# Performance work log

Hardware: AMD Instinct MI355X
Metric: run time of the kernel (lower is better)

The kernel has to match this reference:

```python
import jax, jax.numpy as jnp
from jax import lax
import numpy as np

B, L, CV = 64, 196, 2048
T = 20
VOCAB, E, H, A = 10000, 512, 512, 512


def setup_inputs() -> dict:
    key = jax.random.key(0)
    ks = jax.random.split(key, 16)
    s = 0.02
    return {
        "V": jax.random.normal(ks[0], (B, L, CV), jnp.float32),
        "caps": jax.random.randint(ks[1], (B, T), 0, VOCAB, jnp.int32),
        "embed_W": jax.random.normal(ks[2], (VOCAB, E), jnp.float32) * s,
        "Wh_w": jax.random.normal(ks[3], (A, H), jnp.float32) * s,
        "Wh_b": jnp.zeros((A,), jnp.float32),
        "Wv_w": jax.random.normal(ks[4], (A, CV), jnp.float32) * s,
        "Wv_b": jnp.zeros((A,), jnp.float32),
        "v_w": jax.random.normal(ks[5], (1, A), jnp.float32) * s,
        "v_b": jnp.zeros((1,), jnp.float32),
        "W_ih": jax.random.normal(ks[6], (4 * H, E + CV), jnp.float32) * s,
        "W_hh": jax.random.normal(ks[7], (4 * H, H), jnp.float32) * s,
        "b_ih": jnp.zeros((4 * H,), jnp.float32),
        "b_hh": jnp.zeros((4 * H,), jnp.float32),
        "out_w": jax.random.normal(ks[8], (VOCAB, H), jnp.float32) * s,
        "out_b": jnp.zeros((VOCAB,), jnp.float32),
    }


def reference(V, caps, embed_W, Wh_w, Wh_b, Wv_w, Wv_b, v_w, v_b,
              W_ih, W_hh, b_ih, b_hh, out_w, out_b):
    Bv = V.shape[0]
    Tc = caps.shape[1]
    Hd = W_hh.shape[1]
    emb = embed_W[caps]  # [B,T,E]
    # attention keys over image regions are constant across timesteps
    k = jnp.einsum('blc,ac->bla', V, Wv_w) + Wv_b  # [B,L,A]
    h0 = jnp.zeros((Bv, Hd), V.dtype)
    c0 = jnp.zeros((Bv, Hd), V.dtype)

    def step(carry, yprev):
        h, c = carry
        # additive attention
        q = h @ Wh_w.T + Wh_b                                  # [B,A]
        e = jnp.einsum('bla,a->bl', jnp.tanh(q[:, None, :] + k), v_w[0]) + v_b[0]
        a = jax.nn.softmax(e, axis=-1)                         # [B,L]
        ctx = jnp.einsum('bl,blc->bc', a, V)                   # [B,CV]
        # LSTMCell
        x = jnp.concatenate([yprev, ctx], axis=-1)             # [B,E+CV]
        gates = x @ W_ih.T + b_ih + h @ W_hh.T + b_hh          # [B,4H]
        i, f, g, o = jnp.split(gates, 4, axis=-1)
        c_new = jax.nn.sigmoid(f) * c + jax.nn.sigmoid(i) * jnp.tanh(g)
        h_new = jax.nn.sigmoid(o) * jnp.tanh(c_new)
        logits = h_new @ out_w.T + out_b                       # [B,VOCAB]
        return (h_new, c_new), logits

    xs = jnp.transpose(emb[:, :Tc - 1, :], (1, 0, 2))          # [T-1,B,E]
    _, logits = lax.scan(step, (h0, c0), xs)                   # [T-1,B,VOCAB]
    return jnp.transpose(logits, (1, 0, 2))                    # [B,T-1,VOCAB]
```

## Files before the change

kernel.cpp:

```cpp
#include <hip/hip_runtime.h>


typedef __bf16 bf16x8 __attribute__((ext_vector_type(8)));
typedef float f32x4 __attribute__((ext_vector_type(4)));
typedef unsigned short ushort8 __attribute__((ext_vector_type(8)));

#define OFF_HALL 0ull
#define OFF_X2H  622592ull
#define OFF_H    704512ull
#define OFF_C    737280ull
#define OFF_QP   770048ull
#define OFF_PART 901120ull
#define OFF_AB   1425408ull

#define D_WGH 0ull
#define D_GE  2621440ull
#define D_KB  5111808ull

__device__ __forceinline__ unsigned short f2bf(float f) {
    unsigned int u = __float_as_uint(f);
    unsigned int r = u + 0x7FFFu + ((u >> 16) & 1u);
    return (unsigned short)(r >> 16);
}
__device__ __forceinline__ float bf2f(unsigned short h) {
    return __uint_as_float(((unsigned int)h) << 16);
}
__device__ __forceinline__ float ftanh(float x) {
    x = fminf(fmaxf(x, -15.f), 15.f);
    float e = __expf(2.f * x);
    return (e - 1.f) / (e + 1.f);
}
__device__ __forceinline__ float fsig(float x) {
    x = fminf(fmaxf(x, -30.f), 30.f);
    return 1.f / (1.f + __expf(-x));
}

__global__ void init_state(float* __restrict__ ws) {
    const int b = blockIdx.x, tid = threadIdx.x;
    float* h  = ws + OFF_H;
    float* c  = ws + OFF_C;
    unsigned short* x2h = (unsigned short*)(ws + OFF_X2H);
    for (int j = tid; j < 512; j += 256) {
        h[b * 512 + j] = 0.f;
        c[b * 512 + j] = 0.f;
        x2h[b * 2560 + 2048 + j] = 0;
    }
}

__global__ __launch_bounds__(256)
void conv_wg(const float* __restrict__ Wih, const float* __restrict__ Whh,
             unsigned short* __restrict__ Wgh) {
    const int idx = blockIdx.x * 256 + threadIdx.x;
    const int j = idx / 320;
    const int c0 = (idx - j * 320) * 8;
    const float* src;
    if (c0 < 2048) src = Wih + (size_t)j * 2560 + 512 + c0;
    else           src = Whh + (size_t)j * 512 + (c0 - 2048);
    float4 a = *reinterpret_cast<const float4*>(src);
    float4 b = *reinterpret_cast<const float4*>(src + 4);
    ushort8 o;
    o[0]=f2bf(a.x); o[1]=f2bf(a.y); o[2]=f2bf(a.z); o[3]=f2bf(a.w);
    o[4]=f2bf(b.x); o[5]=f2bf(b.y); o[6]=f2bf(b.z); o[7]=f2bf(b.w);
    *reinterpret_cast<ushort8*>(Wgh + (size_t)j * 2560 + c0) = o;
}

__global__ __launch_bounds__(256)
void gemm_k_mfma(const float* __restrict__ V, const float* __restrict__ Wv,
                 const float* __restrict__ bv, unsigned short* __restrict__ kout) {
    __shared__ unsigned short At[64 * 32];
    __shared__ unsigned short Bt[64 * 32];
    const int tid = threadIdx.x;
    const int lane = tid & 63, wave = tid >> 6;
    const int wr = wave >> 1, wc = wave & 1;
    const int m0 = blockIdx.x * 64, n0 = blockIdx.y * 64;
    const int srow = tid >> 2, skg = tid & 3;
    const float* ga = V  + (size_t)(m0 + srow) * 2048 + skg * 8;
    const float* gb = Wv + (size_t)(n0 + srow) * 2048 + skg * 8;
    const int ar0 = (wr * 32 + (lane & 15)) * 32 + (lane >> 4) * 8;
    const int br0 = (wc * 32 + (lane & 15)) * 32 + (lane >> 4) * 8;
    f32x4 acc[2][2] = {};
    for (int k0 = 0; k0 < 2048; k0 += 32) {
        float4 a0 = *reinterpret_cast<const float4*>(ga + k0);
        float4 a1 = *reinterpret_cast<const float4*>(ga + k0 + 4);
        float4 b0 = *reinterpret_cast<const float4*>(gb + k0);
        float4 b1 = *reinterpret_cast<const float4*>(gb + k0 + 4);
        ushort8 ua, ub;
        ua[0]=f2bf(a0.x); ua[1]=f2bf(a0.y); ua[2]=f2bf(a0.z); ua[3]=f2bf(a0.w);
        ua[4]=f2bf(a1.x); ua[5]=f2bf(a1.y); ua[6]=f2bf(a1.z); ua[7]=f2bf(a1.w);
        ub[0]=f2bf(b0.x); ub[1]=f2bf(b0.y); ub[2]=f2bf(b0.z); ub[3]=f2bf(b0.w);
        ub[4]=f2bf(b1.x); ub[5]=f2bf(b1.y); ub[6]=f2bf(b1.z); ub[7]=f2bf(b1.w);
        *reinterpret_cast<ushort8*>(&At[tid * 8]) = ua;
        *reinterpret_cast<ushort8*>(&Bt[tid * 8]) = ub;
        __syncthreads();
        bf16x8 af0 = *reinterpret_cast<const bf16x8*>(&At[ar0]);
        bf16x8 af1 = *reinterpret_cast<const bf16x8*>(&At[ar0 + 16 * 32]);
        bf16x8 bf0 = *reinterpret_cast<const bf16x8*>(&Bt[br0]);
        bf16x8 bf1 = *reinterpret_cast<const bf16x8*>(&Bt[br0 + 16 * 32]);
        acc[0][0] = __builtin_amdgcn_mfma_f32_16x16x32_bf16(af0, bf0, acc[0][0], 0, 0, 0);
        acc[0][1] = __builtin_amdgcn_mfma_f32_16x16x32_bf16(af0, bf1, acc[0][1], 0, 0, 0);
        acc[1][0] = __builtin_amdgcn_mfma_f32_16x16x32_bf16(af1, bf0, acc[1][0], 0, 0, 0);
        acc[1][1] = __builtin_amdgcn_mfma_f32_16x16x32_bf16(af1, bf1, acc[1][1], 0, 0, 0);
        __syncthreads();
    }
#pragma unroll
    for (int fi = 0; fi < 2; ++fi)
#pragma unroll
        for (int fj = 0; fj < 2; ++fj)
#pragma unroll
            for (int r = 0; r < 4; ++r) {
                int m = m0 + wr * 32 + fi * 16 + (lane >> 4) * 4 + r;
                int n = n0 + wc * 32 + fj * 16 + (lane & 15);
                kout[(size_t)m * 512 + n] = f2bf(acc[fi][fj][r] + bv[n]);
            }
}

__global__ __launch_bounds__(256)
void gemm_emb(const float* __restrict__ embW, const int* __restrict__ caps,
              const float* __restrict__ Wih, const float* __restrict__ bih,
              const float* __restrict__ bhh, float* __restrict__ ge) {
    const int t = blockIdx.x;
    const int n0 = blockIdx.y * 64;
    __shared__ float As[32][68];
    __shared__ float Bs[32][68];
    __shared__ int capss[64];
    const int tid = threadIdx.x;
    const int tx = tid & 15, ty = tid >> 4;
    if (tid < 64) capss[tid] = caps[tid * 20 + t];
    __syncthreads();
    float acc[4][4] = {{0.f}};
    for (int k0 = 0; k0 < 512; k0 += 32) {
#pragma unroll
        for (int i = 0; i < 2; ++i) {
            int idx = tid + i * 256;
            int m = idx >> 3, cc = idx & 7;
            float4 av = *reinterpret_cast<const float4*>(embW + (size_t)capss[m] * 512 + k0 + cc * 4);
            As[cc * 4 + 0][m] = av.x; As[cc * 4 + 1][m] = av.y;
            As[cc * 4 + 2][m] = av.z; As[cc * 4 + 3][m] = av.w;
            float4 bw = *reinterpret_cast<const float4*>(Wih + (size_t)(n0 + m) * 2560 + k0 + cc * 4);
            Bs[cc * 4 + 0][m] = bw.x; Bs[cc * 4 + 1][m] = bw.y;
            Bs[cc * 4 + 2][m] = bw.z; Bs[cc * 4 + 3][m] = bw.w;
        }
        __syncthreads();
#pragma unroll
        for (int kk = 0; kk < 32; ++kk) {
            float4 a4 = *reinterpret_cast<const float4*>(&As[kk][ty * 4]);
            float4 b4 = *reinterpret_cast<const float4*>(&Bs[kk][tx * 4]);
            float ar[4] = {a4.x, a4.y, a4.z, a4.w};
            float br[4] = {b4.x, b4.y, b4.z, b4.w};
#pragma unroll
            for (int i2 = 0; i2 < 4; ++i2)
#pragma unroll
                for (int j2 = 0; j2 < 4; ++j2)
                    acc[i2][j2] = fmaf(ar[i2], br[j2], acc[i2][j2]);
        }
        __syncthreads();
    }
#pragma unroll
    for (int i2 = 0; i2 < 4; ++i2) {
        int m = ty * 4 + i2;
        int n = n0 + tx * 4;
        float4 o;
        o.x = acc[i2][0] + bih[n + 0] + bhh[n + 0];
        o.y = acc[i2][1] + bih[n + 1] + bhh[n + 1];
        o.z = acc[i2][2] + bih[n + 2] + bhh[n + 2];
        o.w = acc[i2][3] + bih[n + 3] + bhh[n + 3];
        *reinterpret_cast<float4*>(ge + (size_t)(t * 64 + m) * 2048 + n) = o;
    }
}

__global__ __launch_bounds__(256)
void kq_gemm(const float* __restrict__ Whw, float* __restrict__ ws) {
    const float* h = ws + OFF_H;
    float* qp = ws + OFF_QP;
    const int n0 = blockIdx.x * 64;
    const int kc = blockIdx.y;
    __shared__ float As[32][68];
    __shared__ float Bs[32][68];
    const int tid = threadIdx.x;
    const int tx = tid & 15, ty = tid >> 4;
    float acc[4][4] = {{0.f}};
    for (int kt = 0; kt < 4; ++kt) {
        int kb = kc * 128 + kt * 32;
#pragma unroll
        for (int i = 0; i < 2; ++i) {
            int idx = tid + i * 256;
            int m = idx >> 3, cc = idx & 7;
            float4 av = *reinterpret_cast<const float4*>(h + (size_t)m * 512 + kb + cc * 4);
            As[cc * 4 + 0][m] = av.x; As[cc * 4 + 1][m] = av.y;
            As[cc * 4 + 2][m] = av.z; As[cc * 4 + 3][m] = av.w;
            float4 bw = *reinterpret_cast<const float4*>(Whw + (size_t)(n0 + m) * 512 + kb + cc * 4);
            Bs[cc * 4 + 0][m] = bw.x; Bs[cc * 4 + 1][m] = bw.y;
            Bs[cc * 4 + 2][m] = bw.z; Bs[cc * 4 + 3][m] = bw.w;
        }
        __syncthreads();
#pragma unroll
        for (int kk = 0; kk < 32; ++kk) {
            float4 a4 = *reinterpret_cast<const float4*>(&As[kk][ty * 4]);
            float4 b4 = *reinterpret_cast<const float4*>(&Bs[kk][tx * 4]);
            float ar[4] = {a4.x, a4.y, a4.z, a4.w};
            float br[4] = {b4.x, b4.y, b4.z, b4.w};
#pragma unroll
            for (int i2 = 0; i2 < 4; ++i2)
#pragma unroll
                for (int j2 = 0; j2 < 4; ++j2)
                    acc[i2][j2] = fmaf(ar[i2], br[j2], acc[i2][j2]);
        }
        __syncthreads();
    }
#pragma unroll
    for (int i2 = 0; i2 < 4; ++i2) {
        int b = ty * 4 + i2;
        int n = n0 + tx * 4;
        float4 o = make_float4(acc[i2][0], acc[i2][1], acc[i2][2], acc[i2][3]);
        *reinterpret_cast<float4*>(qp + (size_t)(kc * 64 + b) * 512 + n) = o;
    }
}

__global__ __launch_bounds__(256)
void attn_step(const float* __restrict__ Whb, const float* __restrict__ vw,
               const unsigned short* __restrict__ kb, float* __restrict__ ws) {
    const int b = blockIdx.x, tid = threadIdx.x;
    const float* qp = ws + OFF_QP;
    float* abuf = ws + OFF_AB;
    __shared__ float qs[512];
    __shared__ float es[196];
    __shared__ float red[256];
    for (int j = tid; j < 512; j += 256) {
        float q = Whb[j];
#pragma unroll
        for (int p = 0; p < 4; ++p) q += qp[(size_t)(p * 64 + b) * 512 + j];
        qs[j] = q;
    }
    __syncthreads();
    const int w = tid >> 6, lane = tid & 63;
    float qr[8], vr[8];
#pragma unroll
    for (int j = 0; j < 8; ++j) {
        qr[j] = qs[lane * 8 + j];
        vr[j] = vw[lane * 8 + j];
    }
    for (int l = w; l < 196; l += 4) {
        const unsigned short* kr = kb + (size_t)(b * 196 + l) * 512 + lane * 8;
        ushort8 kv = *reinterpret_cast<const ushort8*>(kr);
        float s = 0.f;
#pragma unroll
        for (int j = 0; j < 8; ++j)
            s += vr[j] * ftanh(qr[j] + bf2f(kv[j]));
#pragma unroll
        for (int mm = 32; mm >= 1; mm >>= 1) s += __shfl_xor(s, mm);
        if (lane == 0) es[l] = s;
    }
    __syncthreads();
    float ev = (tid < 196) ? es[tid] : -1e30f;
    red[tid] = ev;
    __syncthreads();
    for (int s2 = 128; s2 > 0; s2 >>= 1) {
        if (tid < s2) red[tid] = fmaxf(red[tid], red[tid + s2]);
        __syncthreads();
    }
    float mx = red[0];
    __syncthreads();
    float p = (tid < 196) ? __expf(ev - mx) : 0.f;
    red[tid] = p;
    __syncthreads();
    for (int s2 = 128; s2 > 0; s2 >>= 1) {
        if (tid < s2) red[tid] += red[tid + s2];
        __syncthreads();
    }
    if (tid < 196) abuf[b * 196 + tid] = p / red[0];
}

__global__ __launch_bounds__(256)
void ctx_wide(const float* __restrict__ V, float* __restrict__ ws) {
    const int b = blockIdx.y, tid = threadIdx.x;
    const int c = blockIdx.x * 256 + tid;
    const float* abuf = ws + OFF_AB;
    unsigned short* x2h = (unsigned short*)(ws + OFF_X2H);
    __shared__ float as_[196];
    if (tid < 196) as_[tid] = abuf[b * 196 + tid];
    __syncthreads();
    const float* vb = V + (size_t)b * 196 * 2048 + c;
    float a0 = 0.f, a1 = 0.f, a2 = 0.f, a3 = 0.f;
    for (int l = 0; l < 196; l += 4) {
        a0 = fmaf(as_[l + 0], vb[(size_t)(l + 0) * 2048], a0);
        a1 = fmaf(as_[l + 1], vb[(size_t)(l + 1) * 2048], a1);
        a2 = fmaf(as_[l + 2], vb[(size_t)(l + 2) * 2048], a2);
        a3 = fmaf(as_[l + 3], vb[(size_t)(l + 3) * 2048], a3);
    }
    x2h[(size_t)b * 2560 + c] = f2bf((a0 + a1) + (a2 + a3));
}

__global__ __launch_bounds__(256)
void gates_mfma(const float* __restrict__ ws, const unsigned short* __restrict__ Wgh,
                float* __restrict__ part_out) {
    __shared__ unsigned short At[64 * 32];
    __shared__ unsigned short Bt[64 * 32];
    const unsigned short* x2h = (const unsigned short*)(ws + OFF_X2H);
    const int tid = threadIdx.x;
    const int lane = tid & 63, wave = tid >> 6;
    const int wr = wave >> 1, wc = wave & 1;
    const int n0 = blockIdx.x * 64;
    const int kc = blockIdx.y;
    const int srow = tid >> 2, skg = tid & 3;
    const unsigned short* ga = x2h + (size_t)srow * 2560 + kc * 640 + skg * 8;
    const unsigned short* gb = Wgh + (size_t)(n0 + srow) * 2560 + kc * 640 + skg * 8;
    const int ar0 = (wr * 32 + (lane & 15)) * 32 + (lane >> 4) * 8;
    const int br0 = (wc * 32 + (lane & 15)) * 32 + (lane >> 4) * 8;
    f32x4 acc[2][2] = {};
    for (int kt = 0; kt < 20; ++kt) {
        *reinterpret_cast<ushort8*>(&At[tid * 8]) = *reinterpret_cast<const ushort8*>(ga + kt * 32);
        *reinterpret_cast<ushort8*>(&Bt[tid * 8]) = *reinterpret_cast<const ushort8*>(gb + kt * 32);
        __syncthreads();
        bf16x8 af0 = *reinterpret_cast<const bf16x8*>(&At[ar0]);
        bf16x8 af1 = *reinterpret_cast<const bf16x8*>(&At[ar0 + 16 * 32]);
        bf16x8 bf0 = *reinterpret_cast<const bf16x8*>(&Bt[br0]);
        bf16x8 bf1 = *reinterpret_cast<const bf16x8*>(&Bt[br0 + 16 * 32]);
        acc[0][0] = __builtin_amdgcn_mfma_f32_16x16x32_bf16(af0, bf0, acc[0][0], 0, 0, 0);
        acc[0][1] = __builtin_amdgcn_mfma_f32_16x16x32_bf16(af0, bf1, acc[0][1], 0, 0, 0);
        acc[1][0] = __builtin_amdgcn_mfma_f32_16x16x32_bf16(af1, bf0, acc[1][0], 0, 0, 0);
        acc[1][1] = __builtin_amdgcn_mfma_f32_16x16x32_bf16(af1, bf1, acc[1][1], 0, 0, 0);
        __syncthreads();
    }
#pragma unroll
    for (int fi = 0; fi < 2; ++fi)
#pragma unroll
        for (int fj = 0; fj < 2; ++fj)
#pragma unroll
            for (int r = 0; r < 4; ++r) {
                int m = wr * 32 + fi * 16 + (lane >> 4) * 4 + r;
                int n = n0 + wc * 32 + fj * 16 + (lane & 15);
                part_out[(size_t)(kc * 64 + m) * 2048 + n] = acc[fi][fj][r];
            }
}

__global__ __launch_bounds__(256)
void lstm_step(float* __restrict__ ws, const float* __restrict__ geb, int t) {
    const int b = blockIdx.x, tid = threadIdx.x;
    const float* ge = geb + (size_t)(t * 64 + b) * 2048;
    const float* part = ws + OFF_PART;
    float* h = ws + OFF_H;
    float* c = ws + OFF_C;
    unsigned short* x2h = (unsigned short*)(ws + OFF_X2H);
    float* hall = ws + OFF_HALL;
#pragma unroll
    for (int jj = 0; jj < 2; ++jj) {
        int j = tid + jj * 256;
        float ig = ge[j], fg = ge[512 + j], gg = ge[1024 + j], og = ge[1536 + j];
#pragma unroll
        for (int p = 0; p < 4; ++p) {
            const float* pp = part + (size_t)(p * 64 + b) * 2048;
            ig += pp[j]; fg += pp[512 + j]; gg += pp[1024 + j]; og += pp[1536 + j];
        }
        float cv = fsig(fg) * c[b * 512 + j] + fsig(ig) * ftanh(gg);
        float hv = fsig(og) * ftanh(cv);
        c[b * 512 + j] = cv;
        h[b * 512 + j] = hv;
        x2h[(size_t)b * 2560 + 2048 + j] = f2bf(hv);
        hall[(size_t)(t * 64 + b) * 512 + j] = hv;
    }
}

__global__ __launch_bounds__(256)
void gemm_logits_mfma(const float* __restrict__ outw, const float* __restrict__ outb,
                      const float* __restrict__ ws, float* __restrict__ out) {
    __shared__ unsigned short At[64 * 32];
    __shared__ unsigned short Bt[64 * 32];
    const float* hall = ws + OFF_HALL;
    const int tid = threadIdx.x;
    const int lane = tid & 63, wave = tid >> 6;
    const int wr = wave >> 1, wc = wave & 1;
    const int t = blockIdx.x;
    const int n0 = blockIdx.y * 64;
    const int srow = tid >> 2, skg = tid & 3;
    int brow = n0 + srow; if (brow > 9999) brow = 9999;
    const float* ga = hall + (size_t)(t * 64 + srow) * 512 + skg * 8;
    const float* gb = outw + (size_t)brow * 512 + skg * 8;
    const int ar0 = (wr * 32 + (lane & 15)) * 32 + (lane >> 4) * 8;
    const int br0 = (wc * 32 + (lane & 15)) * 32 + (lane >> 4) * 8;
    f32x4 acc[2][2] = {};
    for (int k0 = 0; k0 < 512; k0 += 32) {
        float4 a0 = *reinterpret_cast<const float4*>(ga + k0);
        float4 a1 = *reinterpret_cast<const float4*>(ga + k0 + 4);
        float4 b0 = *reinterpret_cast<const float4*>(gb + k0);
        float4 b1 = *reinterpret_cast<const float4*>(gb + k0 + 4);
        ushort8 ua, ub;
        ua[0]=f2bf(a0.x); ua[1]=f2bf(a0.y); ua[2]=f2bf(a0.z); ua[3]=f2bf(a0.w);
        ua[4]=f2bf(a1.x); ua[5]=f2bf(a1.y); ua[6]=f2bf(a1.z); ua[7]=f2bf(a1.w);
        ub[0]=f2bf(b0.x); ub[1]=f2bf(b0.y); ub[2]=f2bf(b0.z); ub[3]=f2bf(b0.w);
        ub[4]=f2bf(b1.x); ub[5]=f2bf(b1.y); ub[6]=f2bf(b1.z); ub[7]=f2bf(b1.w);
        *reinterpret_cast<ushort8*>(&At[tid * 8]) = ua;
        *reinterpret_cast<ushort8*>(&Bt[tid * 8]) = ub;
        __syncthreads();
        bf16x8 af0 = *reinterpret_cast<const bf16x8*>(&At[ar0]);
        bf16x8 af1 = *reinterpret_cast<const bf16x8*>(&At[ar0 + 16 * 32]);
        bf16x8 bf0 = *reinterpret_cast<const bf16x8*>(&Bt[br0]);
        bf16x8 bf1 = *reinterpret_cast<const bf16x8*>(&Bt[br0 + 16 * 32]);
        acc[0][0] = __builtin_amdgcn_mfma_f32_16x16x32_bf16(af0, bf0, acc[0][0], 0, 0, 0);
        acc[0][1] = __builtin_amdgcn_mfma_f32_16x16x32_bf16(af0, bf1, acc[0][1], 0, 0, 0);
        acc[1][0] = __builtin_amdgcn_mfma_f32_16x16x32_bf16(af1, bf0, acc[1][0], 0, 0, 0);
        acc[1][1] = __builtin_amdgcn_mfma_f32_16x16x32_bf16(af1, bf1, acc[1][1], 0, 0, 0);
        __syncthreads();
    }
#pragma unroll
    for (int fi = 0; fi < 2; ++fi)
#pragma unroll
        for (int fj = 0; fj < 2; ++fj)
#pragma unroll
            for (int r = 0; r < 4; ++r) {
                int b = wr * 32 + fi * 16 + (lane >> 4) * 4 + r;
                int n = n0 + wc * 32 + fj * 16 + (lane & 15);
                if (n < 10000)
                    out[((size_t)b * 19 + t) * 10000 + n] = acc[fi][fj][r] + outb[n];
            }
}

extern "C" void kernel_launch(void* const* d_in, const int* in_sizes, int n_in,
                              void* d_out, int out_size, void* d_ws, size_t ws_size,
                              hipStream_t stream) {
    const float* V    = (const float*)d_in[0];
    const int*   caps = (const int*)d_in[1];
    const float* embW = (const float*)d_in[2];
    const float* Whw  = (const float*)d_in[3];
    const float* Whb  = (const float*)d_in[4];
    const float* Wvw  = (const float*)d_in[5];
    const float* Wvb  = (const float*)d_in[6];
    const float* vw   = (const float*)d_in[7];
    const float* Wih  = (const float*)d_in[9];
    const float* Whh  = (const float*)d_in[10];
    const float* bih  = (const float*)d_in[11];
    const float* bhh  = (const float*)d_in[12];
    const float* outw = (const float*)d_in[13];
    const float* outb = (const float*)d_in[14];
    float* ws  = (float*)d_ws;
    float* out = (float*)d_out;

    unsigned short* Wgh  = (unsigned short*)(out + D_WGH);
    float*          ge   = out + D_GE;
    unsigned short* kbuf = (unsigned short*)(out + D_KB);
    float*          part = ws + OFF_PART;

    init_state<<<dim3(64), dim3(256), 0, stream>>>(ws);
    conv_wg<<<dim3(2560), dim3(256), 0, stream>>>(Wih, Whh, Wgh);
    gemm_k_mfma<<<dim3(196, 8), dim3(256), 0, stream>>>(V, Wvw, Wvb, kbuf);
    gemm_emb<<<dim3(19, 32), dim3(256), 0, stream>>>(embW, caps, Wih, bih, bhh, ge);

    for (int t = 0; t < 19; ++t) {
        kq_gemm<<<dim3(8, 4), dim3(256), 0, stream>>>(Whw, ws);
        attn_step<<<dim3(64), dim3(256), 0, stream>>>(Whb, vw, kbuf, ws);
        ctx_wide<<<dim3(8, 64), dim3(256), 0, stream>>>(V, ws);
        gates_mfma<<<dim3(32, 4), dim3(256), 0, stream>>>(ws, Wgh, part);
        lstm_step<<<dim3(64), dim3(256), 0, stream>>>(ws, ge, t);
    }

    gemm_logits_mfma<<<dim3(19, 157), dim3(256), 0, stream>>>(outw, outb, ws, out);
}
```

Measured before the change: 1.888 ms.

## Fuse query projection into attention, MFMA embedding GEMM, pre-convert Wv to bf16

Removes the per-step kq_gemm launch by computing h@Wh^T inside each attention block with wave-level dot products and shuffle reductions. The embedding-gate GEMM moves from scalar FMA to bf16 MFMA. Wv is converted to bf16 once, so the key GEMM loads half the bytes for B. Each of the 64 attention blocks now reads the full 1 MB Wh matrix, which adds redundant L2 traffic and a serial q computation in place of one small parallel GEMM launch.

```diff
diff --git a/kernel.cpp b/kernel.cpp
--- a/kernel.cpp
+++ b/kernel.cpp
@@ -16,6 +16,7 @@
 #define D_WGH 0ull
 #define D_GE  2621440ull
 #define D_KB  5111808ull
+#define D_WV  8323072ull
 
 __device__ __forceinline__ unsigned short f2bf(float f) {
     unsigned int u = __float_as_uint(f);
@@ -65,7 +66,18 @@
 }
 
 __global__ __launch_bounds__(256)
-void gemm_k_mfma(const float* __restrict__ V, const float* __restrict__ Wv,
+void conv_wv(const float* __restrict__ Wv, unsigned short* __restrict__ Wvb) {
+    const size_t idx = ((size_t)blockIdx.x * 256 + threadIdx.x) * 8;
+    float4 a = *reinterpret_cast<const float4*>(Wv + idx);
+    float4 b = *reinterpret_cast<const float4*>(Wv + idx + 4);
+    ushort8 o;
+    o[0]=f2bf(a.x); o[1]=f2bf(a.y); o[2]=f2bf(a.z); o[3]=f2bf(a.w);
+    o[4]=f2bf(b.x); o[5]=f2bf(b.y); o[6]=f2bf(b.z); o[7]=f2bf(b.w);
+    *reinterpret_cast<ushort8*>(Wvb + idx) = o;
+}
+
+__global__ __launch_bounds__(256)
+void gemm_k_mfma(const float* __restrict__ V, const unsigned short* __restrict__ Wvb,
                  const float* __restrict__ bv, unsigned short* __restrict__ kout) {
     __shared__ unsigned short At[64 * 32];
     __shared__ unsigned short Bt[64 * 32];
@@ -74,12 +86,62 @@
     const int wr = wave >> 1, wc = wave & 1;
     const int m0 = blockIdx.x * 64, n0 = blockIdx.y * 64;
     const int srow = tid >> 2, skg = tid & 3;
-    const float* ga = V  + (size_t)(m0 + srow) * 2048 + skg * 8;
-    const float* gb = Wv + (size_t)(n0 + srow) * 2048 + skg * 8;
+    const float* ga = V + (size_t)(m0 + srow) * 2048 + skg * 8;
+    const unsigned short* gb = Wvb + (size_t)(n0 + srow) * 2048 + skg * 8;
     const int ar0 = (wr * 32 + (lane & 15)) * 32 + (lane >> 4) * 8;
     const int br0 = (wc * 32 + (lane & 15)) * 32 + (lane >> 4) * 8;
     f32x4 acc[2][2] = {};
     for (int k0 = 0; k0 < 2048; k0 += 32) {
+        float4 a0 = *reinterpret_cast<const float4*>(ga + k0);
+        float4 a1 = *reinterpret_cast<const float4*>(ga + k0 + 4);
+        ushort8 ub = *reinterpret_cast<const ushort8*>(gb + k0);
+        ushort8 ua;
+        ua[0]=f2bf(a0.x); ua[1]=f2bf(a0.y); ua[2]=f2bf(a0.z); ua[3]=f2bf(a0.w);
+        ua[4]=f2bf(a1.x); ua[5]=f2bf(a1.y); ua[6]=f2bf(a1.z); ua[7]=f2bf(a1.w);
+        *reinterpret_cast<ushort8*>(&At[tid * 8]) = ua;
+        *reinterpret_cast<ushort8*>(&Bt[tid * 8]) = ub;
+        __syncthreads();
+        bf16x8 af0 = *reinterpret_cast<const bf16x8*>(&At[ar0]);
+        bf16x8 af1 = *reinterpret_cast<const bf16x8*>(&At[ar0 + 16 * 32]);
+        bf16x8 bf0 = *reinterpret_cast<const bf16x8*>(&Bt[br0]);
+        bf16x8 bf1 = *reinterpret_cast<const bf16x8*>(&Bt[br0 + 16 * 32]);
+        acc[0][0] = __builtin_amdgcn_mfma_f32_16x16x32_bf16(af0, bf0, acc[0][0], 0, 0, 0);
+        acc[0][1] = __builtin_amdgcn_mfma_f32_16x16x32_bf16(af0, bf1, acc[0][1], 0, 0, 0);
+        acc[1][0] = __builtin_amdgcn_mfma_f32_16x16x32_bf16(af1, bf0, acc[1][0], 0, 0, 0);
+        acc[1][1] = __builtin_amdgcn_mfma_f32_16x16x32_bf16(af1, bf1, acc[1][1], 0, 0, 0);
+        __syncthreads();
+    }
+#pragma unroll
+    for (int fi = 0; fi < 2; ++fi)
+#pragma unroll
+        for (int fj = 0; fj < 2; ++fj)
+#pragma unroll
+            for (int r = 0; r < 4; ++r) {
+                int m = m0 + wr * 32 + fi * 16 + (lane >> 4) * 4 + r;
+                int n = n0 + wc * 32 + fj * 16 + (lane & 15);
+                kout[(size_t)m * 512 + n] = f2bf(acc[fi][fj][r] + bv[n]);
+            }
+}
+
+__global__ __launch_bounds__(256)
+void emb_mfma(const float* __restrict__ embW, const int* __restrict__ caps,
+              const float* __restrict__ Wih, const float* __restrict__ bih,
+              const float* __restrict__ bhh, float* __restrict__ ge) {
+    __shared__ unsigned short At[64 * 32];
+    __shared__ unsigned short Bt[64 * 32];
+    const int t = blockIdx.x;
+    const int n0 = blockIdx.y * 64;
+    const int tid = threadIdx.x;
+    const int lane = tid & 63, wave = tid >> 6;
+    const int wr = wave >> 1, wc = wave & 1;
+    const int srow = tid >> 2, skg = tid & 3;
+    const int cap = caps[srow * 20 + t];
+    const float* ga = embW + (size_t)cap * 512 + skg * 8;
+    const float* gb = Wih + (size_t)(n0 + srow) * 2560 + skg * 8;
+    const int ar0 = (wr * 32 + (lane & 15)) * 32 + (lane >> 4) * 8;
+    const int br0 = (wc * 32 + (lane & 15)) * 32 + (lane >> 4) * 8;
+    f32x4 acc[2][2] = {};
+    for (int k0 = 0; k0 < 512; k0 += 32) {
         float4 a0 = *reinterpret_cast<const float4*>(ga + k0);
         float4 a1 = *reinterpret_cast<const float4*>(ga + k0 + 4);
         float4 b0 = *reinterpret_cast<const float4*>(gb + k0);
@@ -108,131 +170,52 @@
         for (int fj = 0; fj < 2; ++fj)
 #pragma unroll
             for (int r = 0; r < 4; ++r) {
-                int m = m0 + wr * 32 + fi * 16 + (lane >> 4) * 4 + r;
+                int m = wr * 32 + fi * 16 + (lane >> 4) * 4 + r;
                 int n = n0 + wc * 32 + fj * 16 + (lane & 15);
-                kout[(size_t)m * 512 + n] = f2bf(acc[fi][fj][r] + bv[n]);
+                ge[(size_t)(t * 64 + m) * 2048 + n] = acc[fi][fj][r] + bih[n] + bhh[n];
             }
 }
 
 __global__ __launch_bounds__(256)
-void gemm_emb(const float* __restrict__ embW, const int* __restrict__ caps,
-              const float* __restrict__ Wih, const float* __restrict__ bih,
-              const float* __restrict__ bhh, float* __restrict__ ge) {
-    const int t = blockIdx.x;
-    const int n0 = blockIdx.y * 64;
-    __shared__ float As[32][68];
-    __shared__ float Bs[32][68];
-    __shared__ int capss[64];
-    const int tid = threadIdx.x;
-    const int tx = tid & 15, ty = tid >> 4;
-    if (tid < 64) capss[tid] = caps[tid * 20 + t];
-    __syncthreads();
-    float acc[4][4] = {{0.f}};
-    for (int k0 = 0; k0 < 512; k0 += 32) {
-#pragma unroll
-        for (int i = 0; i < 2; ++i) {
-            int idx = tid + i * 256;
-            int m = idx >> 3, cc = idx & 7;
-            float4 av = *reinterpret_cast<const float4*>(embW + (size_t)capss[m] * 512 + k0 + cc * 4);
-            As[cc * 4 + 0][m] = av.x; As[cc * 4 + 1][m] = av.y;
-            As[cc * 4 + 2][m] = av.z; As[cc * 4 + 3][m] = av.w;
-            float4 bw = *reinterpret_cast<const float4*>(Wih + (size_t)(n0 + m) * 2560 + k0 + cc * 4);
-            Bs[cc * 4 + 0][m] = bw.x; Bs[cc * 4 + 1][m] = bw.y;
-            Bs[cc * 4 + 2][m] = bw.z; Bs[cc * 4 + 3][m] = bw.w;
-        }
-        __syncthreads();
-#pragma unroll
-        for (int kk = 0; kk < 32; ++kk) {
-            float4 a4 = *reinterpret_cast<const float4*>(&As[kk][ty * 4]);
-            float4 b4 = *reinterpret_cast<const float4*>(&Bs[kk][tx * 4]);
-            float ar[4] = {a4.x, a4.y, a4.z, a4.w};
-            float br[4] = {b4.x, b4.y, b4.z, b4.w};
-#pragma unroll
-            for (int i2 = 0; i2 < 4; ++i2)
-#pragma unroll
-                for (int j2 = 0; j2 < 4; ++j2)
-                    acc[i2][j2] = fmaf(ar[i2], br[j2], acc[i2][j2]);
-        }
-        __syncthreads();
-    }
-#pragma unroll
-    for (int i2 = 0; i2 < 4; ++i2) {
-        int m = ty * 4 + i2;
-        int n = n0 + tx * 4;
-        float4 o;
-        o.x = acc[i2][0] + bih[n + 0] + bhh[n + 0];
-        o.y = acc[i2][1] + bih[n + 1] + bhh[n + 1];
-        o.z = acc[i2][2] + bih[n + 2] + bhh[n + 2];
-        o.w = acc[i2][3] + bih[n + 3] + bhh[n + 3];
-        *reinterpret_cast<float4*>(ge + (size_t)(t * 64 + m) * 2048 + n) = o;
-    }
-}
-
-__global__ __launch_bounds__(256)
-void kq_gemm(const float* __restrict__ Whw, float* __restrict__ ws) {
-    const float* h = ws + OFF_H;
-    float* qp = ws + OFF_QP;
-    const int n0 = blockIdx.x * 64;
-    const int kc = blockIdx.y;
-    __shared__ float As[32][68];
-    __shared__ float Bs[32][68];
-    const int tid = threadIdx.x;
-    const int tx = tid & 15, ty = tid >> 4;
-    float acc[4][4] = {{0.f}};
-    for (int kt = 0; kt < 4; ++kt) {
-        int kb = kc * 128 + kt * 32;
-#pragma unroll
-        for (int i = 0; i < 2; ++i) {
-            int idx = tid + i * 256;
-            int m = idx >> 3, cc = idx & 7;
-            float4 av = *reinterpret_cast<const float4*>(h + (size_t)m * 512 + kb + cc * 4);
-            As[cc * 4 + 0][m] = av.x; As[cc * 4 + 1][m] = av.y;
-            As[cc * 4 + 2][m] = av.z; As[cc * 4 + 3][m] = av.w;
-            float4 bw = *reinterpret_cast<const float4*>(Whw + (size_t)(n0 + m) * 512 + kb + cc * 4);
-            Bs[cc * 4 + 0][m] = bw.x; Bs[cc * 4 + 1][m] = bw.y;
-            Bs[cc * 4 + 2][m] = bw.z; Bs[cc * 4 + 3][m] = bw.w;
-        }
-        __syncthreads();
-#pragma unroll
-        for (int kk = 0; kk < 32; ++kk) {
-            float4 a4 = *reinterpret_cast<const float4*>(&As[kk][ty * 4]);
-            float4 b4 = *reinterpret_cast<const float4*>(&Bs[kk][tx * 4]);
-            float ar[4] = {a4.x, a4.y, a4.z, a4.w};
-            float br[4] = {b4.x, b4.y, b4.z, b4.w};
-#pragma unroll
-            for (int i2 = 0; i2 < 4; ++i2)
-#pragma unroll
-                for (int j2 = 0; j2 < 4; ++j2)
-                    acc[i2][j2] = fmaf(ar[i2], br[j2], acc[i2][j2]);
-        }
-        __syncthreads();
-    }
-#pragma unroll
-    for (int i2 = 0; i2 < 4; ++i2) {
-        int b = ty * 4 + i2;
-        int n = n0 + tx * 4;
-        float4 o = make_float4(acc[i2][0], acc[i2][1], acc[i2][2], acc[i2][3]);
-        *reinterpret_cast<float4*>(qp + (size_t)(kc * 64 + b) * 512 + n) = o;
-    }
-}
-
-__global__ __launch_bounds__(256)
-void attn_step(const float* __restrict__ Whb, const float* __restrict__ vw,
-               const unsigned short* __restrict__ kb, float* __restrict__ ws) {
+void attn_fused(const float* __restrict__ Whw, const float* __restrict__ Whb,
+                const float* __restrict__ vw, const unsigned short* __restrict__ kb,
+                float* __restrict__ ws) {
     const int b = blockIdx.x, tid = threadIdx.x;
-    const float* qp = ws + OFF_QP;
+    const int lane = tid & 63, w = tid >> 6;
+    const float* h = ws + OFF_H + b * 512;
     float* abuf = ws + OFF_AB;
     __shared__ float qs[512];
     __shared__ float es[196];
     __shared__ float red[256];
-    for (int j = tid; j < 512; j += 256) {
-        float q = Whb[j];
-#pragma unroll
-        for (int p = 0; p < 4; ++p) q += qp[(size_t)(p * 64 + b) * 512 + j];
-        qs[j] = q;
-    }
-    __syncthreads();
-    const int w = tid >> 6, lane = tid & 63;
+    float hr[8];
+    {
+        float4 h0 = *reinterpret_cast<const float4*>(h + lane * 8);
+        float4 h1 = *reinterpret_cast<const float4*>(h + lane * 8 + 4);
+        hr[0]=h0.x; hr[1]=h0.y; hr[2]=h0.z; hr[3]=h0.w;
+        hr[4]=h1.x; hr[5]=h1.y; hr[6]=h1.z; hr[7]=h1.w;
+    }
+    for (int j = w * 128; j < w * 128 + 128; j += 2) {
+        const float* w0 = Whw + (size_t)j * 512 + lane * 8;
+        const float* w1 = w0 + 512;
+        float4 a0 = *reinterpret_cast<const float4*>(w0);
+        float4 a1 = *reinterpret_cast<const float4*>(w0 + 4);
+        float4 b0 = *reinterpret_cast<const float4*>(w1);
+        float4 b1 = *reinterpret_cast<const float4*>(w1 + 4);
+        float s0 = hr[0]*a0.x + hr[1]*a0.y + hr[2]*a0.z + hr[3]*a0.w
+                 + hr[4]*a1.x + hr[5]*a1.y + hr[6]*a1.z + hr[7]*a1.w;
+        float s1 = hr[0]*b0.x + hr[1]*b0.y + hr[2]*b0.z + hr[3]*b0.w
+                 + hr[4]*b1.x + hr[5]*b1.y + hr[6]*b1.z + hr[7]*b1.w;
+#pragma unroll
+        for (int mm = 32; mm >= 1; mm >>= 1) {
+            s0 += __shfl_xor(s0, mm);
+            s1 += __shfl_xor(s1, mm);
+        }
+        if (lane == 0) {
+            qs[j]     = s0 + Whb[j];
+            qs[j + 1] = s1 + Whb[j + 1];
+        }
+    }
+    __syncthreads();
     float qr[8], vr[8];
 #pragma unroll
     for (int j = 0; j < 8; ++j) {
@@ -434,19 +417,20 @@
     float* ws  = (float*)d_ws;
     float* out = (float*)d_out;
 
-    unsigned short* Wgh  = (unsigned short*)(out + D_WGH);
-    float*          ge   = out + D_GE;
-    unsigned short* kbuf = (unsigned short*)(out + D_KB);
-    float*          part = ws + OFF_PART;
+    unsigned short* Wgh   = (unsigned short*)(out + D_WGH);
+    float*          ge    = out + D_GE;
+    unsigned short* kbuf  = (unsigned short*)(out + D_KB);
+    unsigned short* Wvbf  = (unsigned short*)(out + D_WV);
+    float*          part  = ws + OFF_PART;
 
     init_state<<<dim3(64), dim3(256), 0, stream>>>(ws);
     conv_wg<<<dim3(2560), dim3(256), 0, stream>>>(Wih, Whh, Wgh);
-    gemm_k_mfma<<<dim3(196, 8), dim3(256), 0, stream>>>(V, Wvw, Wvb, kbuf);
-    gemm_emb<<<dim3(19, 32), dim3(256), 0, stream>>>(embW, caps, Wih, bih, bhh, ge);
+    conv_wv<<<dim3(512), dim3(256), 0, stream>>>(Wvw, Wvbf);
+    gemm_k_mfma<<<dim3(196, 8), dim3(256), 0, stream>>>(V, Wvbf, Wvb, kbuf);
+    emb_mfma<<<dim3(19, 32), dim3(256), 0, stream>>>(embW, caps, Wih, bih, bhh, ge);
 
     for (int t = 0; t < 19; ++t) {
-        kq_gemm<<<dim3(8, 4), dim3(256), 0, stream>>>(Whw, ws);
-        attn_step<<<dim3(64), dim3(256), 0, stream>>>(Whb, vw, kbuf, ws);
+        attn_fused<<<dim3(64), dim3(256), 0, stream>>>(Whw, Whb, vw, kbuf, ws);
         ctx_wide<<<dim3(8, 64), dim3(256), 0, stream>>>(V, ws);
         gates_mfma<<<dim3(32, 4), dim3(256), 0, stream>>>(ws, Wgh, part);
         lstm_step<<<dim3(64), dim3(256), 0, stream>>>(ws, ge, t);
```

Result: slower. 2.474 ms (+31.0%).
